# Optimization experiments

Measured on AMD Instinct MI355X. Metric: run time of the kernel, lower is better.

The kernel has to match this reference:

```python
import jax, jax.numpy as jnp
import numpy as np

N, L, H, E = 4, 4096, 8, 64
CHUNK = 128  # chunk size for the blocked causal scan
EPS = 1e-6


def elu_feature_map(x):
    # phi(x) = elu(x) + 1 (default feature map of fast-transformers)
    return jax.nn.elu(x) + 1.0


def causal_dot_product(Q, K, V, chunk=CHUNK):
    """out[n,l,h,:] = sum_{s<=l} (Q[n,l,h,:].K[n,s,h,:]) * V[n,s,h,:].
    Chunked scan over the [E,M] KV state: O(N L H E M) without an [L,L] matrix."""
    n, l, h, e = Q.shape
    m = V.shape[-1]
    nc = l // chunk

    def to_chunks(x):
        # [n, l, h, d] -> [nc, n, h, chunk, d]
        return x.reshape(n, nc, chunk, h, x.shape[-1]).transpose(1, 0, 3, 2, 4)

    q, k, v = to_chunks(Q), to_chunks(K), to_chunks(V)
    tril = jnp.tril(jnp.ones((chunk, chunk), dtype=Q.dtype))

    def step(S, xs):  # S: [n, h, e, m] running sum of k v^T
        qc, kc, vc = xs  # [n, h, chunk, e/m]
        inter = jnp.einsum('nhce,nhem->nhcm', qc, S)
        attn = jnp.einsum('nhce,nhde->nhcd', qc, kc) * tril  # intra-chunk causal
        intra = jnp.einsum('nhcd,nhdm->nhcm', attn, vc)
        S = S + jnp.einsum('nhce,nhcm->nhem', kc, vc)
        return S, inter + intra

    S0 = jnp.zeros((n, h, e, m), dtype=Q.dtype)
    _, out = jax.lax.scan(step, S0, (q, k, v))  # [nc, n, h, chunk, m]
    return out.transpose(1, 0, 3, 2, 4).reshape(n, l, h, m)


def setup_inputs() -> dict:
    key = jax.random.key(0)
    k1, k2, k3 = jax.random.split(key, 3)
    return {
        'queries': jax.random.normal(k1, (N, L, H, E), jnp.float32),
        'keys': jax.random.normal(k2, (N, L, H, E), jnp.float32),
        'values': jax.random.normal(k3, (N, L, H, E), jnp.float32),
        'key_lengths': jnp.ones((N, L), jnp.float32),  # float length mask
    }


def reference(queries, keys, values, key_lengths):
    Q = elu_feature_map(queries)
    K = elu_feature_map(keys) * key_lengths[:, :, None, None]
    # denominator: Z[n,l,h] = 1 / (Q[n,l,h] . cumsum_s<=l K[n,s,h] + eps)
    Z = 1.0 / (jnp.einsum('nlhe,nlhe->nlh', Q, jnp.cumsum(K, axis=1)) + EPS)
    V_new = causal_dot_product(Q, K, values)
    return V_new * Z[:, :, :, None]
```

## Files before the change

kernel.cpp:

```cpp
#include <hip/hip_runtime.h>
#include <math.h>

#define NN 4
#define LL 4096
#define HH 8
#define EE 64
#define CHK 64
#define GSUP 4
#define NSUP 16
#define NH (NN*HH)
#define NBLK (NH*NSUP)
#define NCH64 (LL/CHK)
#define EPSF 1e-6f

typedef float f32x4 __attribute__((ext_vector_type(4)));
typedef __bf16 bf16x8 __attribute__((ext_vector_type(8)));
typedef __bf16 bf16x4 __attribute__((ext_vector_type(4)));

__device__ __forceinline__ float phi_map(float x) {
  return x > 0.0f ? x + 1.0f : __expf(x);
}

#define MFMA(a, b, c) __builtin_amdgcn_mfma_f32_16x16x32_bf16((a), (b), (c), 0, 0, 0)

__device__ __forceinline__ int swz64(int row, int d) {
  return row * 64 + (d & 7) + 8 * ((d >> 3) ^ ((row >> 2) & 7));
}
__device__ __forceinline__ int frag64(int row, int blk) {
  return row * 64 + 8 * (blk ^ ((row >> 2) & 7));
}

#define K1_ISSUE(J, BUF) { \
  const int l0i = (sc * GSUP + (J)) * CHK; \
  _Pragma("unroll") for (int it = 0; it < 4; ++it) { \
    int f = t + 256 * it; int d = f >> 4; int c4 = (f & 15) << 2; \
    size_t gb = (((size_t)n * LL + (size_t)(l0i + d)) * HH + h) * EE + c4; \
    pk[BUF][it] = *(const float4*)(Kg + gb); \
    pv[BUF][it] = *(const float4*)(Vg + gb); \
    pl[BUF][it] = KLg[n * LL + l0i + d]; } }

#define K1_STAGE(BUF) { \
  _Pragma("unroll") for (int it = 0; it < 4; ++it) { \
    int f = t + 256 * it; int d = f >> 4; int c4 = (f & 15) << 2; \
    float klr = pl[BUF][it]; float4 kk = pk[BUF][it]; float4 vv = pv[BUF][it]; \
    float ka[4] = {phi_map(kk.x) * klr, phi_map(kk.y) * klr, phi_map(kk.z) * klr, phi_map(kk.w) * klr}; \
    float va[4] = {vv.x, vv.y, vv.z, vv.w}; \
    _Pragma("unroll") for (int jj = 0; jj < 4; ++jj) { \
      sKt[BUF][swz64(c4 + jj, d)] = (__bf16)ka[jj]; \
      sVt[BUF][swz64(c4 + jj, d)] = (__bf16)va[jj]; } } }

__global__ __launch_bounds__(256, 2) void k_chunksums(
    const float* __restrict__ Kg, const float* __restrict__ Vg,
    const float* __restrict__ KLg, __bf16* __restrict__ ScG, __bf16* __restrict__ KscG)
{
  __shared__ __bf16 sKt[2][4096];
  __shared__ __bf16 sVt[2][4096];
  const int g = blockIdx.x;
  const int sc = g & (NSUP - 1);
  const int nh = g >> 4;
  const int h = nh % HH;
  const int n = nh / HH;
  const int t = threadIdx.x;
  const int w = t >> 6;
  const int lane = t & 63;
  const int lg = lane >> 4;
  const int li = lane & 15;
  const int arow = 16 * w + li;

  float4 pk[2][4], pv[2][4];
  float pl[2][4];

  K1_ISSUE(0, 0);
  K1_STAGE(0);

  f32x4 acc[4];
  #pragma unroll
  for (int nt = 0; nt < 4; ++nt) acc[nt] = (f32x4){0.f, 0.f, 0.f, 0.f};

  bf16x8 ones;
  #pragma unroll
  for (int i = 0; i < 8; ++i) ones[i] = (__bf16)1.0f;

  #pragma unroll
  for (int j = 0; j < GSUP; ++j) {
    if (j + 1 < GSUP) K1_ISSUE(j + 1, (j + 1) & 1);
    __syncthreads();

    bf16x8 bV0 = *(const bf16x8*)&sVt[j & 1][frag64(arow, lg)];
    bf16x8 bV1 = *(const bf16x8*)&sVt[j & 1][frag64(arow, 4 + lg)];

    f32x4 accK[4];
    #pragma unroll
    for (int nt = 0; nt < 4; ++nt) accK[nt] = (f32x4){0.f, 0.f, 0.f, 0.f};

    #pragma unroll
    for (int nt = 0; nt < 4; ++nt) {
      bf16x8 a0 = *(const bf16x8*)&sKt[j & 1][frag64(li + 16 * nt, lg)];
      bf16x8 a1 = *(const bf16x8*)&sKt[j & 1][frag64(li + 16 * nt, 4 + lg)];
      acc[nt] = MFMA(a0, bV0, acc[nt]);
      acc[nt] = MFMA(a1, bV1, acc[nt]);
      if (w == 0) {
        accK[nt] = MFMA(ones, a0, accK[nt]);
        accK[nt] = MFMA(ones, a1, accK[nt]);
      }
    }
    if (w == 0 && lg == 0) {
      #pragma unroll
      for (int nt = 0; nt < 4; ++nt)
        KscG[(size_t)(g * GSUP + j) * 64 + li + 16 * nt] = (__bf16)accK[nt][0];
    }
    if (j + 1 < GSUP) K1_STAGE((j + 1) & 1);
  }

  __bf16* sp = ScG + (size_t)g * 4096;
  #pragma unroll
  for (int nt = 0; nt < 4; ++nt) {
    bf16x4 sv;
    #pragma unroll
    for (int reg = 0; reg < 4; ++reg) sv[reg] = (__bf16)acc[nt][reg];
    *(bf16x4*)(sp + arow * 64 + 16 * nt + 4 * lg) = sv;
  }
}

__global__ __launch_bounds__(256) void k_prefix(
    __bf16* __restrict__ Sc, __bf16* __restrict__ Ksc)
{
  const int bid = blockIdx.x;
  const int t = threadIdx.x;
  if (bid < NH * 16) {
    const int nh = bid >> 4;
    const int strip = bid & 15;
    const int entry = strip * 256 + t;
    __bf16 v[NSUP];
    #pragma unroll
    for (int c = 0; c < NSUP; ++c)
      v[c] = Sc[((size_t)(nh * NSUP + c) << 12) + entry];
    float run = 0.0f;
    #pragma unroll
    for (int c = 0; c < NSUP; ++c) {
      Sc[((size_t)(nh * NSUP + c) << 12) + entry] = (__bf16)run;
      run += (float)v[c];
    }
  } else {
    const int idx = (bid - NH * 16) * 256 + t;
    const int nh = idx >> 6;
    const int e = idx & 63;
    __bf16 v[NCH64];
    #pragma unroll
    for (int c = 0; c < NCH64; ++c)
      v[c] = Ksc[((size_t)(nh * NCH64 + c) << 6) + e];
    float run = 0.0f;
    #pragma unroll
    for (int c = 0; c < NCH64; ++c) {
      Ksc[((size_t)(nh * NCH64 + c) << 6) + e] = (__bf16)run;
      run += (float)v[c];
    }
  }
}

__global__ __launch_bounds__(512, 1) void k_pass2(
    const float* __restrict__ Qg, const float* __restrict__ Kg,
    const float* __restrict__ Vg, const float* __restrict__ KLg,
    const __bf16* __restrict__ Sp, const __bf16* __restrict__ Ksp,
    float* __restrict__ Og)
{
  __shared__ __bf16 sKe[2][4096];
  __shared__ __bf16 sKt[2][4096];
  __shared__ __bf16 sVt[2][4096];
  __shared__ __bf16 sU[2][4096];
  __shared__ __bf16 sP[4][1024];

  const int g = blockIdx.x;
  const int sc = g & (NSUP - 1);
  const int nh = g >> 4;
  const int h = nh % HH;
  const int n = nh / HH;
  const int t = threadIdx.x;
  const int w = t >> 6;
  const int lane = t & 63;
  const int lg = lane >> 4;
  const int li = lane & 15;
  const int cw = w & 3;
  const int arow = 16 * cw + li;
  const int t2 = t & 255;

  f32x4 accS[4];
  float4 pq[4];

  if (w >= 4) {
    const int l0i = sc * GSUP * CHK;
    #pragma unroll
    for (int it = 0; it < 4; ++it) {
      int f = t2 + 256 * it; int d = f >> 4; int c4 = (f & 15) << 2;
      size_t gb = (((size_t)n * LL + (size_t)(l0i + d)) * HH + h) * EE + c4;
      float4 kk = *(const float4*)(Kg + gb);
      float4 vv = *(const float4*)(Vg + gb);
      float klr = KLg[n * LL + l0i + d];
      float ka[4] = {phi_map(kk.x) * klr, phi_map(kk.y) * klr,
                     phi_map(kk.z) * klr, phi_map(kk.w) * klr};
      float va[4] = {vv.x, vv.y, vv.z, vv.w};
      bf16x4 kv4;
      kv4[0] = (__bf16)ka[0]; kv4[1] = (__bf16)ka[1];
      kv4[2] = (__bf16)ka[2]; kv4[3] = (__bf16)ka[3];
      *(bf16x4*)&sKe[0][d * 64 + 8 * ((c4 >> 3) ^ ((d >> 2) & 7)) + (c4 & 7)] = kv4;
      #pragma unroll
      for (int jj = 0; jj < 4; ++jj) {
        sKt[0][swz64(c4 + jj, d)] = (__bf16)ka[jj];
        sVt[0][swz64(c4 + jj, d)] = (__bf16)va[jj];
      }
    }
  } else {
    {
      const bf16x8* sp8 = (const bf16x8*)(Sp + (size_t)g * 4096);
      bf16x8 s0 = sp8[2 * t];
      bf16x8 s1 = sp8[2 * t + 1];
      int m = t >> 2, eb = (t & 3) * 2;
      *(bf16x8*)&sU[0][frag64(m, eb)] = s0;
      *(bf16x8*)&sU[0][frag64(m, eb + 1)] = s1;
    }
    #pragma unroll
    for (int nt = 0; nt < 4; ++nt) {
      bf16x4 sv = *(const bf16x4*)(Sp + (size_t)g * 4096 + arow * 64 + 16 * nt + 4 * lg);
      #pragma unroll
      for (int reg = 0; reg < 4; ++reg) accS[nt][reg] = (float)sv[reg];
    }
    {
      const float* qr = Qg + (((size_t)n * LL + (size_t)(sc * GSUP * CHK + arow)) * HH + h) * EE;
      pq[0] = *(const float4*)(qr + 8 * lg);
      pq[1] = *(const float4*)(qr + 8 * lg + 4);
      pq[2] = *(const float4*)(qr + 32 + 8 * lg);
      pq[3] = *(const float4*)(qr + 32 + 8 * lg + 4);
    }
  }
  __syncthreads();

  #pragma unroll
  for (int cc = 0; cc < GSUP; ++cc) {
    const int cb = cc & 1, nb = cb ^ 1;

    if (w < 4) {
      bf16x8 aQ0, aQ1;
      {
        float4 q0 = pq[0], q1 = pq[1], q2 = pq[2], q3 = pq[3];
        aQ0[0] = (__bf16)phi_map(q0.x); aQ0[1] = (__bf16)phi_map(q0.y);
        aQ0[2] = (__bf16)phi_map(q0.z); aQ0[3] = (__bf16)phi_map(q0.w);
        aQ0[4] = (__bf16)phi_map(q1.x); aQ0[5] = (__bf16)phi_map(q1.y);
        aQ0[6] = (__bf16)phi_map(q1.z); aQ0[7] = (__bf16)phi_map(q1.w);
        aQ1[0] = (__bf16)phi_map(q2.x); aQ1[1] = (__bf16)phi_map(q2.y);
        aQ1[2] = (__bf16)phi_map(q2.z); aQ1[3] = (__bf16)phi_map(q2.w);
        aQ1[4] = (__bf16)phi_map(q3.x); aQ1[5] = (__bf16)phi_map(q3.y);
        aQ1[6] = (__bf16)phi_map(q3.z); aQ1[7] = (__bf16)phi_map(q3.w);
      }
      if (cc + 1 < GSUP) {
        const float* qr = Qg + (((size_t)n * LL +
            (size_t)((sc * GSUP + cc + 1) * CHK + arow)) * HH + h) * EE;
        pq[0] = *(const float4*)(qr + 8 * lg);
        pq[1] = *(const float4*)(qr + 8 * lg + 4);
        pq[2] = *(const float4*)(qr + 32 + 8 * lg);
        pq[3] = *(const float4*)(qr + 32 + 8 * lg + 4);
      }

      const __bf16* kb = Ksp + (size_t)(g * GSUP + cc) * 64;
      bf16x8 ks0 = *(const bf16x8*)(kb + 8 * lg);
      bf16x8 ks1 = *(const bf16x8*)(kb + 32 + 8 * lg);

      f32x4 acc[4];
      #pragma unroll
      for (int nt = 0; nt < 4; ++nt) {
        acc[nt] = (f32x4){0.f, 0.f, 0.f, 0.f};
        bf16x8 aS0 = *(const bf16x8*)&sU[cb][frag64(li + 16 * nt, lg)];
        bf16x8 aS1 = *(const bf16x8*)&sU[cb][frag64(li + 16 * nt, 4 + lg)];
        acc[nt] = MFMA(aS0, aQ0, acc[nt]);
        acc[nt] = MFMA(aS1, aQ1, acc[nt]);
      }

      float dv = 0.0f;
      #pragma unroll
      for (int i = 0; i < 8; ++i) {
        dv += (float)aQ0[i] * (float)ks0[i];
        dv += (float)aQ1[i] * (float)ks1[i];
      }
      dv += __shfl_xor(dv, 16);
      dv += __shfl_xor(dv, 32);

      f32x4 at2[4];
      #pragma unroll
      for (int nt = 0; nt < 4; ++nt) at2[nt] = (f32x4){0.f, 0.f, 0.f, 0.f};
      for (int nt = 0; nt <= cw; ++nt) {
        bf16x8 aK0 = *(const bf16x8*)&sKe[cb][frag64(li + 16 * nt, lg)];
        bf16x8 aK1 = *(const bf16x8*)&sKe[cb][frag64(li + 16 * nt, 4 + lg)];
        at2[nt] = MFMA(aK0, aQ0, at2[nt]);
        at2[nt] = MFMA(aK1, aQ1, at2[nt]);
      }

      float rs = 0.0f;
      #pragma unroll
      for (int nt = 0; nt < 4; ++nt) {
        bf16x4 pw;
        #pragma unroll
        for (int reg = 0; reg < 4; ++reg) {
          int kk = 16 * nt + 4 * lg + reg;
          float av = (kk <= arow) ? at2[nt][reg] : 0.0f;
          rs += av;
          pw[reg] = (__bf16)av;
        }
        *(bf16x4*)&sP[cw][li * 64 + 8 * ((2 * nt + (lg >> 1)) ^ (li & 7)) + 4 * (lg & 1)] = pw;
      }
      rs += __shfl_xor(rs, 16);
      rs += __shfl_xor(rs, 32);

      {
        bf16x8 bP0 = *(const bf16x8*)&sP[cw][li * 64 + 8 * (lg ^ (li & 7))];
        bf16x8 bP1 = *(const bf16x8*)&sP[cw][li * 64 + 8 * ((4 + lg) ^ (li & 7))];
        #pragma unroll
        for (int nt = 0; nt < 4; ++nt) {
          bf16x8 aV0 = *(const bf16x8*)&sVt[cb][frag64(li + 16 * nt, lg)];
          bf16x8 aV1 = *(const bf16x8*)&sVt[cb][frag64(li + 16 * nt, 4 + lg)];
          acc[nt] = MFMA(aV0, bP0, acc[nt]);
          acc[nt] = MFMA(aV1, bP1, acc[nt]);
        }
      }

      const int l0 = (sc * GSUP + cc) * CHK;
      {
        float inv = 1.0f / (dv + rs + EPSF);
        size_t ob = (((size_t)n * LL + (size_t)(l0 + arow)) * HH + h) * EE;
        #pragma unroll
        for (int nt = 0; nt < 4; ++nt) {
          float4 o = make_float4(acc[nt][0] * inv, acc[nt][1] * inv,
                                 acc[nt][2] * inv, acc[nt][3] * inv);
          *(float4*)(Og + ob + 16 * nt + 4 * lg) = o;
        }
      }

      if (cc + 1 < GSUP) {
        bf16x8 bV0 = *(const bf16x8*)&sVt[cb][frag64(arow, lg)];
        bf16x8 bV1 = *(const bf16x8*)&sVt[cb][frag64(arow, 4 + lg)];
        #pragma unroll
        for (int nt = 0; nt < 4; ++nt) {
          bf16x8 aKt0 = *(const bf16x8*)&sKt[cb][frag64(li + 16 * nt, lg)];
          bf16x8 aKt1 = *(const bf16x8*)&sKt[cb][frag64(li + 16 * nt, 4 + lg)];
          accS[nt] = MFMA(aKt0, bV0, accS[nt]);
          accS[nt] = MFMA(aKt1, bV1, accS[nt]);
          bf16x4 sw;
          #pragma unroll
          for (int reg = 0; reg < 4; ++reg) sw[reg] = (__bf16)accS[nt][reg];
          *(bf16x4*)&sU[nb][arow * 64 + 8 * ((2 * nt + (lg >> 1)) ^ ((arow >> 2) & 7)) + 4 * (lg & 1)] = sw;
        }
      }
    } else if (cc + 1 < GSUP) {
      const int l0i = (sc * GSUP + cc + 1) * CHK;
      #pragma unroll
      for (int it = 0; it < 4; ++it) {
        int f = t2 + 256 * it; int d = f >> 4; int c4 = (f & 15) << 2;
        size_t gb = (((size_t)n * LL + (size_t)(l0i + d)) * HH + h) * EE + c4;
        float4 kk = *(const float4*)(Kg + gb);
        float4 vv = *(const float4*)(Vg + gb);
        float klr = KLg[n * LL + l0i + d];
        float ka[4] = {phi_map(kk.x) * klr, phi_map(kk.y) * klr,
                       phi_map(kk.z) * klr, phi_map(kk.w) * klr};
        float va[4] = {vv.x, vv.y, vv.z, vv.w};
        bf16x4 kv4;
        kv4[0] = (__bf16)ka[0]; kv4[1] = (__bf16)ka[1];
        kv4[2] = (__bf16)ka[2]; kv4[3] = (__bf16)ka[3];
        *(bf16x4*)&sKe[nb][d * 64 + 8 * ((c4 >> 3) ^ ((d >> 2) & 7)) + (c4 & 7)] = kv4;
        #pragma unroll
        for (int jj = 0; jj < 4; ++jj) {
          sKt[nb][swz64(c4 + jj, d)] = (__bf16)ka[jj];
          sVt[nb][swz64(c4 + jj, d)] = (__bf16)va[jj];
        }
      }
    }
    __syncthreads();
  }
}

extern "C" void kernel_launch(void* const* d_in, const int* in_sizes, int n_in,
                              void* d_out, int out_size, void* d_ws, size_t ws_size,
                              hipStream_t stream) {
  const float* Qg  = (const float*)d_in[0];
  const float* Kg  = (const float*)d_in[1];
  const float* Vg  = (const float*)d_in[2];
  const float* KLg = (const float*)d_in[3];
  float* Og = (float*)d_out;

  __bf16* Sc  = (__bf16*)d_ws;
  __bf16* Ksc = (__bf16*)((char*)d_ws + (size_t)NBLK * 4096 * 2);

  hipLaunchKernelGGL(k_chunksums, dim3(NBLK), dim3(256), 0, stream, Kg, Vg, KLg, Sc, Ksc);
  hipLaunchKernelGGL(k_prefix, dim3(NH * 16 + 8), dim3(256), 0, stream, Sc, Ksc);
  hipLaunchKernelGGL(k_pass2, dim3(NBLK), dim3(512), 0, stream, Qg, Kg, Vg, KLg, Sc, Ksc, Og);
}
```

Measured before the change: 50.49 us.

## Drop super-chunk grouping: one block per 64-row chunk in all passes

Removes the four-chunk super-chunk grouping, so each block handles a single 64-row chunk in both the chunk-sum and output kernels. The grid grows from 512 to 2048 blocks. The intra-block state update and the producer/consumer warp specialization in pass2 go away, and pass2 drops to 256 threads. The prefix scan now runs over 64 chunk states instead of 16. This aims for more parallelism and less serialization per block, at the cost of writing and reading four times as many bf16 state matrices and a longer prefix-scan chain.

```diff
diff --git a/kernel.cpp b/kernel.cpp
--- a/kernel.cpp
+++ b/kernel.cpp
@@ -6,11 +6,9 @@
 #define HH 8
 #define EE 64
 #define CHK 64
-#define GSUP 4
-#define NSUP 16
+#define NCH64 (LL/CHK)
 #define NH (NN*HH)
-#define NBLK (NH*NSUP)
-#define NCH64 (LL/CHK)
+#define NBLK (NH*NCH64)
 #define EPSF 1e-6f
 
 typedef float f32x4 __attribute__((ext_vector_type(4)));
@@ -29,37 +27,19 @@
 __device__ __forceinline__ int frag64(int row, int blk) {
   return row * 64 + 8 * (blk ^ ((row >> 2) & 7));
 }
-
-#define K1_ISSUE(J, BUF) { \
-  const int l0i = (sc * GSUP + (J)) * CHK; \
-  _Pragma("unroll") for (int it = 0; it < 4; ++it) { \
-    int f = t + 256 * it; int d = f >> 4; int c4 = (f & 15) << 2; \
-    size_t gb = (((size_t)n * LL + (size_t)(l0i + d)) * HH + h) * EE + c4; \
-    pk[BUF][it] = *(const float4*)(Kg + gb); \
-    pv[BUF][it] = *(const float4*)(Vg + gb); \
-    pl[BUF][it] = KLg[n * LL + l0i + d]; } }
-
-#define K1_STAGE(BUF) { \
-  _Pragma("unroll") for (int it = 0; it < 4; ++it) { \
-    int f = t + 256 * it; int d = f >> 4; int c4 = (f & 15) << 2; \
-    float klr = pl[BUF][it]; float4 kk = pk[BUF][it]; float4 vv = pv[BUF][it]; \
-    float ka[4] = {phi_map(kk.x) * klr, phi_map(kk.y) * klr, phi_map(kk.z) * klr, phi_map(kk.w) * klr}; \
-    float va[4] = {vv.x, vv.y, vv.z, vv.w}; \
-    _Pragma("unroll") for (int jj = 0; jj < 4; ++jj) { \
-      sKt[BUF][swz64(c4 + jj, d)] = (__bf16)ka[jj]; \
-      sVt[BUF][swz64(c4 + jj, d)] = (__bf16)va[jj]; } } }
 
 __global__ __launch_bounds__(256, 2) void k_chunksums(
     const float* __restrict__ Kg, const float* __restrict__ Vg,
     const float* __restrict__ KLg, __bf16* __restrict__ ScG, __bf16* __restrict__ KscG)
 {
-  __shared__ __bf16 sKt[2][4096];
-  __shared__ __bf16 sVt[2][4096];
+  __shared__ __bf16 sKt[4096];
+  __shared__ __bf16 sVt[4096];
   const int g = blockIdx.x;
-  const int sc = g & (NSUP - 1);
-  const int nh = g >> 4;
+  const int c = g & 63;
+  const int nh = g >> 6;
   const int h = nh % HH;
   const int n = nh / HH;
+  const int l0 = c * CHK;
   const int t = threadIdx.x;
   const int w = t >> 6;
   const int lane = t & 63;
@@ -67,49 +47,50 @@
   const int li = lane & 15;
   const int arow = 16 * w + li;
 
-  float4 pk[2][4], pv[2][4];
-  float pl[2][4];
-
-  K1_ISSUE(0, 0);
-  K1_STAGE(0);
-
-  f32x4 acc[4];
-  #pragma unroll
-  for (int nt = 0; nt < 4; ++nt) acc[nt] = (f32x4){0.f, 0.f, 0.f, 0.f};
+  #pragma unroll
+  for (int it = 0; it < 4; ++it) {
+    int f = t + 256 * it;
+    int d = f >> 4;
+    int c4 = (f & 15) << 2;
+    size_t gb = (((size_t)n * LL + (size_t)(l0 + d)) * HH + h) * EE + c4;
+    float4 kk = *(const float4*)(Kg + gb);
+    float4 vv = *(const float4*)(Vg + gb);
+    float klr = KLg[n * LL + l0 + d];
+    float ka[4] = {phi_map(kk.x) * klr, phi_map(kk.y) * klr,
+                   phi_map(kk.z) * klr, phi_map(kk.w) * klr};
+    float va[4] = {vv.x, vv.y, vv.z, vv.w};
+    #pragma unroll
+    for (int jj = 0; jj < 4; ++jj) {
+      sKt[swz64(c4 + jj, d)] = (__bf16)ka[jj];
+      sVt[swz64(c4 + jj, d)] = (__bf16)va[jj];
+    }
+  }
+  __syncthreads();
 
   bf16x8 ones;
   #pragma unroll
   for (int i = 0; i < 8; ++i) ones[i] = (__bf16)1.0f;
 
-  #pragma unroll
-  for (int j = 0; j < GSUP; ++j) {
-    if (j + 1 < GSUP) K1_ISSUE(j + 1, (j + 1) & 1);
-    __syncthreads();
-
-    bf16x8 bV0 = *(const bf16x8*)&sVt[j & 1][frag64(arow, lg)];
-    bf16x8 bV1 = *(const bf16x8*)&sVt[j & 1][frag64(arow, 4 + lg)];
-
-    f32x4 accK[4];
-    #pragma unroll
-    for (int nt = 0; nt < 4; ++nt) accK[nt] = (f32x4){0.f, 0.f, 0.f, 0.f};
-
-    #pragma unroll
-    for (int nt = 0; nt < 4; ++nt) {
-      bf16x8 a0 = *(const bf16x8*)&sKt[j & 1][frag64(li + 16 * nt, lg)];
-      bf16x8 a1 = *(const bf16x8*)&sKt[j & 1][frag64(li + 16 * nt, 4 + lg)];
-      acc[nt] = MFMA(a0, bV0, acc[nt]);
-      acc[nt] = MFMA(a1, bV1, acc[nt]);
-      if (w == 0) {
-        accK[nt] = MFMA(ones, a0, accK[nt]);
-        accK[nt] = MFMA(ones, a1, accK[nt]);
-      }
-    }
-    if (w == 0 && lg == 0) {
-      #pragma unroll
-      for (int nt = 0; nt < 4; ++nt)
-        KscG[(size_t)(g * GSUP + j) * 64 + li + 16 * nt] = (__bf16)accK[nt][0];
-    }
-    if (j + 1 < GSUP) K1_STAGE((j + 1) & 1);
+  bf16x8 bV0 = *(const bf16x8*)&sVt[frag64(arow, lg)];
+  bf16x8 bV1 = *(const bf16x8*)&sVt[frag64(arow, 4 + lg)];
+
+  f32x4 acc[4], accK[4];
+  #pragma unroll
+  for (int nt = 0; nt < 4; ++nt) {
+    acc[nt] = (f32x4){0.f, 0.f, 0.f, 0.f};
+    accK[nt] = (f32x4){0.f, 0.f, 0.f, 0.f};
+  }
+
+  #pragma unroll
+  for (int nt = 0; nt < 4; ++nt) {
+    bf16x8 a0 = *(const bf16x8*)&sKt[frag64(li + 16 * nt, lg)];
+    bf16x8 a1 = *(const bf16x8*)&sKt[frag64(li + 16 * nt, 4 + lg)];
+    acc[nt] = MFMA(a0, bV0, acc[nt]);
+    acc[nt] = MFMA(a1, bV1, acc[nt]);
+    if (w == 0) {
+      accK[nt] = MFMA(ones, a0, accK[nt]);
+      accK[nt] = MFMA(ones, a1, accK[nt]);
+    }
   }
 
   __bf16* sp = ScG + (size_t)g * 4096;
@@ -119,6 +100,11 @@
     #pragma unroll
     for (int reg = 0; reg < 4; ++reg) sv[reg] = (__bf16)acc[nt][reg];
     *(bf16x4*)(sp + arow * 64 + 16 * nt + 4 * lg) = sv;
+  }
+  if (w == 0 && lg == 0) {
+    #pragma unroll
+    for (int nt = 0; nt < 4; ++nt)
+      KscG[(size_t)g * 64 + li + 16 * nt] = (__bf16)accK[nt][0];
   }
 }
 
@@ -131,14 +117,14 @@
     const int nh = bid >> 4;
     const int strip = bid & 15;
     const int entry = strip * 256 + t;
-    __bf16 v[NSUP];
-    #pragma unroll
-    for (int c = 0; c < NSUP; ++c)
-      v[c] = Sc[((size_t)(nh * NSUP + c) << 12) + entry];
+    __bf16 v[NCH64];
+    #pragma unroll
+    for (int c = 0; c < NCH64; ++c)
+      v[c] = Sc[((size_t)(nh * NCH64 + c) << 12) + entry];
     float run = 0.0f;
     #pragma unroll
-    for (int c = 0; c < NSUP; ++c) {
-      Sc[((size_t)(nh * NSUP + c) << 12) + entry] = (__bf16)run;
+    for (int c = 0; c < NCH64; ++c) {
+      Sc[((size_t)(nh * NCH64 + c) << 12) + entry] = (__bf16)run;
       run += (float)v[c];
     }
   } else {
@@ -158,220 +144,158 @@
   }
 }
 
-__global__ __launch_bounds__(512, 1) void k_pass2(
+__global__ __launch_bounds__(256, 2) void k_pass2(
     const float* __restrict__ Qg, const float* __restrict__ Kg,
     const float* __restrict__ Vg, const float* __restrict__ KLg,
     const __bf16* __restrict__ Sp, const __bf16* __restrict__ Ksp,
     float* __restrict__ Og)
 {
-  __shared__ __bf16 sKe[2][4096];
-  __shared__ __bf16 sKt[2][4096];
-  __shared__ __bf16 sVt[2][4096];
-  __shared__ __bf16 sU[2][4096];
+  __shared__ __bf16 sKe[4096];
+  __shared__ __bf16 sVt[4096];
   __shared__ __bf16 sP[4][1024];
 
   const int g = blockIdx.x;
-  const int sc = g & (NSUP - 1);
-  const int nh = g >> 4;
+  const int c = g & 63;
+  const int nh = g >> 6;
   const int h = nh % HH;
   const int n = nh / HH;
+  const int l0 = c * CHK;
   const int t = threadIdx.x;
   const int w = t >> 6;
   const int lane = t & 63;
   const int lg = lane >> 4;
   const int li = lane & 15;
-  const int cw = w & 3;
-  const int arow = 16 * cw + li;
-  const int t2 = t & 255;
-
-  f32x4 accS[4];
-  float4 pq[4];
-
-  if (w >= 4) {
-    const int l0i = sc * GSUP * CHK;
-    #pragma unroll
-    for (int it = 0; it < 4; ++it) {
-      int f = t2 + 256 * it; int d = f >> 4; int c4 = (f & 15) << 2;
-      size_t gb = (((size_t)n * LL + (size_t)(l0i + d)) * HH + h) * EE + c4;
-      float4 kk = *(const float4*)(Kg + gb);
-      float4 vv = *(const float4*)(Vg + gb);
-      float klr = KLg[n * LL + l0i + d];
-      float ka[4] = {phi_map(kk.x) * klr, phi_map(kk.y) * klr,
-                     phi_map(kk.z) * klr, phi_map(kk.w) * klr};
-      float va[4] = {vv.x, vv.y, vv.z, vv.w};
-      bf16x4 kv4;
-      kv4[0] = (__bf16)ka[0]; kv4[1] = (__bf16)ka[1];
-      kv4[2] = (__bf16)ka[2]; kv4[3] = (__bf16)ka[3];
-      *(bf16x4*)&sKe[0][d * 64 + 8 * ((c4 >> 3) ^ ((d >> 2) & 7)) + (c4 & 7)] = kv4;
-      #pragma unroll
-      for (int jj = 0; jj < 4; ++jj) {
-        sKt[0][swz64(c4 + jj, d)] = (__bf16)ka[jj];
-        sVt[0][swz64(c4 + jj, d)] = (__bf16)va[jj];
-      }
-    }
-  } else {
-    {
-      const bf16x8* sp8 = (const bf16x8*)(Sp + (size_t)g * 4096);
-      bf16x8 s0 = sp8[2 * t];
-      bf16x8 s1 = sp8[2 * t + 1];
-      int m = t >> 2, eb = (t & 3) * 2;
-      *(bf16x8*)&sU[0][frag64(m, eb)] = s0;
-      *(bf16x8*)&sU[0][frag64(m, eb + 1)] = s1;
-    }
+  const int arow = 16 * w + li;
+
+  float4 pk[4], pv[4], pq[4];
+  float pl[4];
+  #pragma unroll
+  for (int it = 0; it < 4; ++it) {
+    int f = t + 256 * it;
+    int d = f >> 4;
+    int c4 = (f & 15) << 2;
+    size_t gb = (((size_t)n * LL + (size_t)(l0 + d)) * HH + h) * EE + c4;
+    pk[it] = *(const float4*)(Kg + gb);
+    pv[it] = *(const float4*)(Vg + gb);
+    pl[it] = KLg[n * LL + l0 + d];
+  }
+  {
+    const float* qr = Qg + (((size_t)n * LL + (size_t)(l0 + arow)) * HH + h) * EE;
+    pq[0] = *(const float4*)(qr + 8 * lg);
+    pq[1] = *(const float4*)(qr + 8 * lg + 4);
+    pq[2] = *(const float4*)(qr + 32 + 8 * lg);
+    pq[3] = *(const float4*)(qr + 32 + 8 * lg + 4);
+  }
+  bf16x8 aS0[4], aS1[4];
+  #pragma unroll
+  for (int nt = 0; nt < 4; ++nt) {
+    const __bf16* srow = Sp + (size_t)g * 4096 + (li + 16 * nt) * 64;
+    aS0[nt] = *(const bf16x8*)(srow + 8 * lg);
+    aS1[nt] = *(const bf16x8*)(srow + 32 + 8 * lg);
+  }
+  const __bf16* kb = Ksp + (size_t)g * 64;
+  bf16x8 ks0 = *(const bf16x8*)(kb + 8 * lg);
+  bf16x8 ks1 = *(const bf16x8*)(kb + 32 + 8 * lg);
+
+  #pragma unroll
+  for (int it = 0; it < 4; ++it) {
+    int f = t + 256 * it;
+    int d = f >> 4;
+    int c4 = (f & 15) << 2;
+    float klr = pl[it];
+    float4 kk = pk[it];
+    float4 vv = pv[it];
+    float ka[4] = {phi_map(kk.x) * klr, phi_map(kk.y) * klr,
+                   phi_map(kk.z) * klr, phi_map(kk.w) * klr};
+    float va[4] = {vv.x, vv.y, vv.z, vv.w};
+    bf16x4 kv4;
+    kv4[0] = (__bf16)ka[0]; kv4[1] = (__bf16)ka[1];
+    kv4[2] = (__bf16)ka[2]; kv4[3] = (__bf16)ka[3];
+    *(bf16x4*)&sKe[d * 64 + 8 * ((c4 >> 3) ^ ((d >> 2) & 7)) + (c4 & 7)] = kv4;
+    #pragma unroll
+    for (int jj = 0; jj < 4; ++jj)
+      sVt[swz64(c4 + jj, d)] = (__bf16)va[jj];
+  }
+
+  bf16x8 aQ0, aQ1;
+  {
+    float4 q0 = pq[0], q1 = pq[1], q2 = pq[2], q3 = pq[3];
+    aQ0[0] = (__bf16)phi_map(q0.x); aQ0[1] = (__bf16)phi_map(q0.y);
+    aQ0[2] = (__bf16)phi_map(q0.z); aQ0[3] = (__bf16)phi_map(q0.w);
+    aQ0[4] = (__bf16)phi_map(q1.x); aQ0[5] = (__bf16)phi_map(q1.y);
+    aQ0[6] = (__bf16)phi_map(q1.z); aQ0[7] = (__bf16)phi_map(q1.w);
+    aQ1[0] = (__bf16)phi_map(q2.x); aQ1[1] = (__bf16)phi_map(q2.y);
+    aQ1[2] = (__bf16)phi_map(q2.z); aQ1[3] = (__bf16)phi_map(q2.w);
+    aQ1[4] = (__bf16)phi_map(q3.x); aQ1[5] = (__bf16)phi_map(q3.y);
+    aQ1[6] = (__bf16)phi_map(q3.z); aQ1[7] = (__bf16)phi_map(q3.w);
+  }
+
+  __syncthreads();
+
+  f32x4 acc[4];
+  #pragma unroll
+  for (int nt = 0; nt < 4; ++nt) {
+    acc[nt] = (f32x4){0.f, 0.f, 0.f, 0.f};
+    acc[nt] = MFMA(aS0[nt], aQ0, acc[nt]);
+    acc[nt] = MFMA(aS1[nt], aQ1, acc[nt]);
+  }
+
+  float dv = 0.0f;
+  #pragma unroll
+  for (int i = 0; i < 8; ++i) {
+    dv += (float)aQ0[i] * (float)ks0[i];
+    dv += (float)aQ1[i] * (float)ks1[i];
+  }
+  dv += __shfl_xor(dv, 16);
+  dv += __shfl_xor(dv, 32);
+
+  f32x4 at2[4];
+  #pragma unroll
+  for (int nt = 0; nt < 4; ++nt) at2[nt] = (f32x4){0.f, 0.f, 0.f, 0.f};
+  for (int nt = 0; nt <= w; ++nt) {
+    bf16x8 aK0 = *(const bf16x8*)&sKe[frag64(li + 16 * nt, lg)];
+    bf16x8 aK1 = *(const bf16x8*)&sKe[frag64(li + 16 * nt, 4 + lg)];
+    at2[nt] = MFMA(aK0, aQ0, at2[nt]);
+    at2[nt] = MFMA(aK1, aQ1, at2[nt]);
+  }
+
+  float rs = 0.0f;
+  #pragma unroll
+  for (int nt = 0; nt < 4; ++nt) {
+    bf16x4 pw;
+    #pragma unroll
+    for (int reg = 0; reg < 4; ++reg) {
+      int kk = 16 * nt + 4 * lg + reg;
+      float av = (kk <= arow) ? at2[nt][reg] : 0.0f;
+      rs += av;
+      pw[reg] = (__bf16)av;
+    }
+    *(bf16x4*)&sP[w][li * 64 + 8 * ((2 * nt + (lg >> 1)) ^ (li & 7)) + 4 * (lg & 1)] = pw;
+  }
+  rs += __shfl_xor(rs, 16);
+  rs += __shfl_xor(rs, 32);
+
+  {
+    bf16x8 bP0 = *(const bf16x8*)&sP[w][li * 64 + 8 * (lg ^ (li & 7))];
+    bf16x8 bP1 = *(const bf16x8*)&sP[w][li * 64 + 8 * ((4 + lg) ^ (li & 7))];
     #pragma unroll
     for (int nt = 0; nt < 4; ++nt) {
-      bf16x4 sv = *(const bf16x4*)(Sp + (size_t)g * 4096 + arow * 64 + 16 * nt + 4 * lg);
-      #pragma unroll
-      for (int reg = 0; reg < 4; ++reg) accS[nt][reg] = (float)sv[reg];
-    }
-    {
-      const float* qr = Qg + (((size_t)n * LL + (size_t)(sc * GSUP * CHK + arow)) * HH + h) * EE;
-      pq[0] = *(const float4*)(qr + 8 * lg);
-      pq[1] = *(const float4*)(qr + 8 * lg + 4);
-      pq[2] = *(const float4*)(qr + 32 + 8 * lg);
-      pq[3] = *(const float4*)(qr + 32 + 8 * lg + 4);
-    }
-  }
-  __syncthreads();
-
-  #pragma unroll
-  for (int cc = 0; cc < GSUP; ++cc) {
-    const int cb = cc & 1, nb = cb ^ 1;
-
-    if (w < 4) {
-      bf16x8 aQ0, aQ1;
-      {
-        float4 q0 = pq[0], q1 = pq[1], q2 = pq[2], q3 = pq[3];
-        aQ0[0] = (__bf16)phi_map(q0.x); aQ0[1] = (__bf16)phi_map(q0.y);
-        aQ0[2] = (__bf16)phi_map(q0.z); aQ0[3] = (__bf16)phi_map(q0.w);
-        aQ0[4] = (__bf16)phi_map(q1.x); aQ0[5] = (__bf16)phi_map(q1.y);
-        aQ0[6] = (__bf16)phi_map(q1.z); aQ0[7] = (__bf16)phi_map(q1.w);
-        aQ1[0] = (__bf16)phi_map(q2.x); aQ1[1] = (__bf16)phi_map(q2.y);
-        aQ1[2] = (__bf16)phi_map(q2.z); aQ1[3] = (__bf16)phi_map(q2.w);
-        aQ1[4] = (__bf16)phi_map(q3.x); aQ1[5] = (__bf16)phi_map(q3.y);
-        aQ1[6] = (__bf16)phi_map(q3.z); aQ1[7] = (__bf16)phi_map(q3.w);
-      }
-      if (cc + 1 < GSUP) {
-        const float* qr = Qg + (((size_t)n * LL +
-            (size_t)((sc * GSUP + cc + 1) * CHK + arow)) * HH + h) * EE;
-        pq[0] = *(const float4*)(qr + 8 * lg);
-        pq[1] = *(const float4*)(qr + 8 * lg + 4);
-        pq[2] = *(const float4*)(qr + 32 + 8 * lg);
-        pq[3] = *(const float4*)(qr + 32 + 8 * lg + 4);
-      }
-
-      const __bf16* kb = Ksp + (size_t)(g * GSUP + cc) * 64;
-      bf16x8 ks0 = *(const bf16x8*)(kb + 8 * lg);
-      bf16x8 ks1 = *(const bf16x8*)(kb + 32 + 8 * lg);
-
-      f32x4 acc[4];
-      #pragma unroll
-      for (int nt = 0; nt < 4; ++nt) {
-        acc[nt] = (f32x4){0.f, 0.f, 0.f, 0.f};
-        bf16x8 aS0 = *(const bf16x8*)&sU[cb][frag64(li + 16 * nt, lg)];
-        bf16x8 aS1 = *(const bf16x8*)&sU[cb][frag64(li + 16 * nt, 4 + lg)];
-        acc[nt] = MFMA(aS0, aQ0, acc[nt]);
-        acc[nt] = MFMA(aS1, aQ1, acc[nt]);
-      }
-
-      float dv = 0.0f;
-      #pragma unroll
-      for (int i = 0; i < 8; ++i) {
-        dv += (float)aQ0[i] * (float)ks0[i];
-        dv += (float)aQ1[i] * (float)ks1[i];
-      }
-      dv += __shfl_xor(dv, 16);
-      dv += __shfl_xor(dv, 32);
-
-      f32x4 at2[4];
-      #pragma unroll
-      for (int nt = 0; nt < 4; ++nt) at2[nt] = (f32x4){0.f, 0.f, 0.f, 0.f};
-      for (int nt = 0; nt <= cw; ++nt) {
-        bf16x8 aK0 = *(const bf16x8*)&sKe[cb][frag64(li + 16 * nt, lg)];
-        bf16x8 aK1 = *(const bf16x8*)&sKe[cb][frag64(li + 16 * nt, 4 + lg)];
-        at2[nt] = MFMA(aK0, aQ0, at2[nt]);
-        at2[nt] = MFMA(aK1, aQ1, at2[nt]);
-      }
-
-      float rs = 0.0f;
-      #pragma unroll
-      for (int nt = 0; nt < 4; ++nt) {
-        bf16x4 pw;
-        #pragma unroll
-        for (int reg = 0; reg < 4; ++reg) {
-          int kk = 16 * nt + 4 * lg + reg;
-          float av = (kk <= arow) ? at2[nt][reg] : 0.0f;
-          rs += av;
-          pw[reg] = (__bf16)av;
-        }
-        *(bf16x4*)&sP[cw][li * 64 + 8 * ((2 * nt + (lg >> 1)) ^ (li & 7)) + 4 * (lg & 1)] = pw;
-      }
-      rs += __shfl_xor(rs, 16);
-      rs += __shfl_xor(rs, 32);
-
-      {
-        bf16x8 bP0 = *(const bf16x8*)&sP[cw][li * 64 + 8 * (lg ^ (li & 7))];
-        bf16x8 bP1 = *(const bf16x8*)&sP[cw][li * 64 + 8 * ((4 + lg) ^ (li & 7))];
-        #pragma unroll
-        for (int nt = 0; nt < 4; ++nt) {
-          bf16x8 aV0 = *(const bf16x8*)&sVt[cb][frag64(li + 16 * nt, lg)];
-          bf16x8 aV1 = *(const bf16x8*)&sVt[cb][frag64(li + 16 * nt, 4 + lg)];
-          acc[nt] = MFMA(aV0, bP0, acc[nt]);
-          acc[nt] = MFMA(aV1, bP1, acc[nt]);
-        }
-      }
-
-      const int l0 = (sc * GSUP + cc) * CHK;
-      {
-        float inv = 1.0f / (dv + rs + EPSF);
-        size_t ob = (((size_t)n * LL + (size_t)(l0 + arow)) * HH + h) * EE;
-        #pragma unroll
-        for (int nt = 0; nt < 4; ++nt) {
-          float4 o = make_float4(acc[nt][0] * inv, acc[nt][1] * inv,
-                                 acc[nt][2] * inv, acc[nt][3] * inv);
-          *(float4*)(Og + ob + 16 * nt + 4 * lg) = o;
-        }
-      }
-
-      if (cc + 1 < GSUP) {
-        bf16x8 bV0 = *(const bf16x8*)&sVt[cb][frag64(arow, lg)];
-        bf16x8 bV1 = *(const bf16x8*)&sVt[cb][frag64(arow, 4 + lg)];
-        #pragma unroll
-        for (int nt = 0; nt < 4; ++nt) {
-          bf16x8 aKt0 = *(const bf16x8*)&sKt[cb][frag64(li + 16 * nt, lg)];
-          bf16x8 aKt1 = *(const bf16x8*)&sKt[cb][frag64(li + 16 * nt, 4 + lg)];
-          accS[nt] = MFMA(aKt0, bV0, accS[nt]);
-          accS[nt] = MFMA(aKt1, bV1, accS[nt]);
-          bf16x4 sw;
-          #pragma unroll
-          for (int reg = 0; reg < 4; ++reg) sw[reg] = (__bf16)accS[nt][reg];
-          *(bf16x4*)&sU[nb][arow * 64 + 8 * ((2 * nt + (lg >> 1)) ^ ((arow >> 2) & 7)) + 4 * (lg & 1)] = sw;
-        }
-      }
-    } else if (cc + 1 < GSUP) {
-      const int l0i = (sc * GSUP + cc + 1) * CHK;
-      #pragma unroll
-      for (int it = 0; it < 4; ++it) {
-        int f = t2 + 256 * it; int d = f >> 4; int c4 = (f & 15) << 2;
-        size_t gb = (((size_t)n * LL + (size_t)(l0i + d)) * HH + h) * EE + c4;
-        float4 kk = *(const float4*)(Kg + gb);
-        float4 vv = *(const float4*)(Vg + gb);
-        float klr = KLg[n * LL + l0i + d];
-        float ka[4] = {phi_map(kk.x) * klr, phi_map(kk.y) * klr,
-                       phi_map(kk.z) * klr, phi_map(kk.w) * klr};
-        float va[4] = {vv.x, vv.y, vv.z, vv.w};
-        bf16x4 kv4;
-        kv4[0] = (__bf16)ka[0]; kv4[1] = (__bf16)ka[1];
-        kv4[2] = (__bf16)ka[2]; kv4[3] = (__bf16)ka[3];
-        *(bf16x4*)&sKe[nb][d * 64 + 8 * ((c4 >> 3) ^ ((d >> 2) & 7)) + (c4 & 7)] = kv4;
-        #pragma unroll
-        for (int jj = 0; jj < 4; ++jj) {
-          sKt[nb][swz64(c4 + jj, d)] = (__bf16)ka[jj];
-          sVt[nb][swz64(c4 + jj, d)] = (__bf16)va[jj];
-        }
-      }
-    }
-    __syncthreads();
+      bf16x8 aV0 = *(const bf16x8*)&sVt[frag64(li + 16 * nt, lg)];
+      bf16x8 aV1 = *(const bf16x8*)&sVt[frag64(li + 16 * nt, 4 + lg)];
+      acc[nt] = MFMA(aV0, bP0, acc[nt]);
+      acc[nt] = MFMA(aV1, bP1, acc[nt]);
+    }
+  }
+
+  {
+    float inv = 1.0f / (dv + rs + EPSF);
+    size_t ob = (((size_t)n * LL + (size_t)(l0 + arow)) * HH + h) * EE;
+    #pragma unroll
+    for (int nt = 0; nt < 4; ++nt) {
+      float4 o = make_float4(acc[nt][0] * inv, acc[nt][1] * inv,
+                             acc[nt][2] * inv, acc[nt][3] * inv);
+      *(float4*)(Og + ob + 16 * nt + 4 * lg) = o;
+    }
   }
 }
 
@@ -389,5 +313,5 @@
 
   hipLaunchKernelGGL(k_chunksums, dim3(NBLK), dim3(256), 0, stream, Kg, Vg, KLg, Sc, Ksc);
   hipLaunchKernelGGL(k_prefix, dim3(NH * 16 + 8), dim3(256), 0, stream, Sc, Ksc);
-  hipLaunchKernelGGL(k_pass2, dim3(NBLK), dim3(512), 0, stream, Qg, Kg, Vg, KLg, Sc, Ksc, Og);
-}
+  hipLaunchKernelGGL(k_pass2, dim3(NBLK), dim3(256), 0, stream, Qg, Kg, Vg, KLg, Sc, Ksc, Og);
+}
```

Measured after the change: 53.43 us. 1.06x slower.
